# Performance work log

Measured on AMD Instinct MI355X. Metric: run time of the kernel, lower is better.

Reference implementation:

```python
import jax, jax.numpy as jnp
import numpy as np

DIM = 256
NUM_HEADS = 8
HEAD_DIM = DIM // NUM_HEADS
KERNEL_SIZES = (5, 7, 9)
DILATIONS = (1, 2, 3)
HEADS_PER_RANGE = (4, 3, 1)  # replicates torch allocation: weights~1/k^2, floor + greedy remainder
SCALE = HEAD_DIM ** -0.5


def _unfold(x, ks, dil):
    # x: (B, h, d, H, W) -> (B, h, d, L, H, W), L = ks*ks, same-padded dilated neighborhood gather
    B, h, d, H, W = x.shape
    pad = (ks // 2) * dil
    xp = jnp.pad(x, ((0, 0), (0, 0), (0, 0), (pad, pad), (pad, pad)))
    patches = [xp[..., i * dil:i * dil + H, j * dil:j * dil + W]
               for i in range(ks) for j in range(ks)]
    return jnp.stack(patches, axis=3)


def _attend_range(q, k, v, ks, dil, rpb):
    # q,k,v: (B, h_i, d, H, W); rpb: (h_i, L)
    k_nb = _unfold(k, ks, dil)  # (B,h,d,L,H,W)
    v_nb = _unfold(v, ks, dil)
    logits = jnp.einsum('bhdxy,bhdlxy->bhlxy', q * SCALE, k_nb)
    logits = logits + rpb[None, :, :, None, None]
    attn = jax.nn.softmax(logits, axis=2)
    return jnp.einsum('bhlxy,bhdlxy->bhdxy', attn, v_nb)


def setup_inputs() -> dict:
    key = jax.random.key(0)
    ks = jax.random.split(key, 6)
    B, C, H, W = 4, DIM, 64, 64
    s = 0.02
    inp = {
        'x': jax.random.normal(ks[0], (B, C, H, W), dtype=jnp.float32),
        'qkv_w': jax.random.normal(ks[1], (3 * DIM, DIM), dtype=jnp.float32) * s,
        'qkv_b': jnp.zeros((3 * DIM,), dtype=jnp.float32),
        'proj_w': jax.random.normal(ks[2], (DIM, DIM), dtype=jnp.float32) * s,
        'proj_b': jnp.zeros((DIM,), dtype=jnp.float32),
    }
    for i, kk in enumerate(KERNEL_SIZES):
        inp[f'rpb{i}'] = jax.random.normal(ks[3 + i], (HEADS_PER_RANGE[i], kk * kk), dtype=jnp.float32) * s
    return inp


def reference(x, qkv_w, qkv_b, proj_w, proj_b, rpb0, rpb1, rpb2):
    B, C, H, W = x.shape
    qkv = jnp.einsum('oc,bcxy->boxy', qkv_w, x) + qkv_b[None, :, None, None]
    q, k, v = jnp.split(qkv, 3, axis=1)
    q = q.reshape(B, NUM_HEADS, HEAD_DIM, H, W)
    k = k.reshape(B, NUM_HEADS, HEAD_DIM, H, W)
    v = v.reshape(B, NUM_HEADS, HEAD_DIM, H, W)
    rpbs = (rpb0, rpb1, rpb2)
    outs = []
    hs = 0
    for i in range(len(KERNEL_SIZES)):
        he = hs + HEADS_PER_RANGE[i]
        outs.append(_attend_range(q[:, hs:he], k[:, hs:he], v[:, hs:he],
                                  KERNEL_SIZES[i], DILATIONS[i], rpbs[i]))
        hs = he
    out = jnp.concatenate(outs, axis=1).reshape(B, C, H, W)
    out = jnp.einsum('oc,bcxy->boxy', proj_w, out) + proj_b[None, :, None, None]
    return out
```

## Files before the change

kernel.cpp:

```cpp
#include <hip/hip_runtime.h>
#include <math.h>

#define H_IMG 64
#define W_IMG 64
#define PIX   (H_IMG * W_IMG)
#define NB    4
#define NHEADS 8
#define HD    32
#define CDIM  256
#define QKV_C 768
#define ATT_SCALE 0.17677669529663687f

typedef _Float16 half8_t __attribute__((ext_vector_type(8)));
typedef _Float16 half2_t __attribute__((ext_vector_type(2)));
typedef float f32x4 __attribute__((ext_vector_type(4)));

__global__ void cvt_w16(const float* __restrict__ a, int na,
                        const float* __restrict__ b, int nb,
                        _Float16* __restrict__ da, _Float16* __restrict__ db) {
    int i = blockIdx.x * 256 + threadIdx.x;
    if (i < na) da[i] = (_Float16)a[i];
    else if (i - na < nb) db[i - na] = (_Float16)b[i - na];
}

__launch_bounds__(256)
__global__ void transpose_to_f16(const float* __restrict__ src,
                                 _Float16* __restrict__ dst, int C) {
    __shared__ _Float16 tl[64][66];
    const int b  = blockIdx.z;
    const int p0 = blockIdx.x * 64;
    const int c0 = blockIdx.y * 64;
    const int tx = threadIdx.x;
    const int ty = threadIdx.y;
    const float* s = src + (size_t)b * C * PIX;
    _Float16* d = dst + (size_t)b * PIX * C;
#pragma unroll
    for (int cc = ty; cc < 64; cc += 4)
        tl[cc][tx] = (_Float16)s[(size_t)(c0 + cc) * PIX + p0 + tx];
    __syncthreads();
#pragma unroll
    for (int pp = ty; pp < 64; pp += 4)
        d[(size_t)(p0 + pp) * C + c0 + tx] = tl[tx][pp];
}

template <typename OutT, bool PAIR>
__launch_bounds__(256)
__global__ void gemm16(const _Float16* __restrict__ A,
                       const _Float16* __restrict__ BT,
                       const float* __restrict__ bias,
                       OutT* __restrict__ Y,
                       int M, int K, int N) {
    __shared__ _Float16 Asl[128][40];
    __shared__ _Float16 Bsl[128][40];
    const int b = blockIdx.z;
    const _Float16* Bb = BT + (size_t)b * N * K;
    OutT* Yb = Y + (size_t)b * M * N;
    const int m0 = blockIdx.y * 128;
    const int n0 = blockIdx.x * 128;
    const int t    = threadIdx.x;
    const int lane = t & 63;
    const int w    = t >> 6;
    const int wm = w >> 1, wn = w & 1;
    const int l15 = lane & 15;
    const int kq  = (lane >> 4) * 8;

    f32x4 acc[4][4];
#pragma unroll
    for (int mt = 0; mt < 4; mt++)
#pragma unroll
        for (int nt = 0; nt < 4; nt++)
            acc[mt][nt] = (f32x4){0.f, 0.f, 0.f, 0.f};

    for (int k0 = 0; k0 < K; k0 += 32) {
        __syncthreads();
#pragma unroll
        for (int i = 0; i < 2; i++) {
            int idx = t + i * 256;
            int row = idx >> 2;
            int seg = (idx & 3) * 8;
            *(half8_t*)&Asl[row][seg] = *(const half8_t*)(A  + (size_t)(m0 + row) * K + k0 + seg);
            *(half8_t*)&Bsl[row][seg] = *(const half8_t*)(Bb + (size_t)(n0 + row) * K + k0 + seg);
        }
        __syncthreads();
        half8_t af[4], bf[4];
#pragma unroll
        for (int mt = 0; mt < 4; mt++)
            af[mt] = *(const half8_t*)&Asl[wm * 64 + mt * 16 + l15][kq];
#pragma unroll
        for (int nt = 0; nt < 4; nt++)
            bf[nt] = *(const half8_t*)&Bsl[wn * 64 + nt * 16 + l15][kq];
#pragma unroll
        for (int mt = 0; mt < 4; mt++)
#pragma unroll
            for (int nt = 0; nt < 4; nt++)
                acc[mt][nt] = __builtin_amdgcn_mfma_f32_16x16x32_f16(
                    af[mt], bf[nt], acc[mt][nt], 0, 0, 0);
    }

    const int rq = lane >> 4;
    if constexpr (PAIR) {
        unsigned* Yp = (unsigned*)Yb;
#pragma unroll
        for (int mt = 0; mt < 4; mt++) {
#pragma unroll
            for (int s = 0; s < 2; s++) {
                int mp = m0 + wm * 64 + mt * 16 + rq * 4 + 2 * s;
                float b0 = bias[mp], b1 = bias[mp + 1];
#pragma unroll
                for (int nt = 0; nt < 4; nt++) {
                    int col = n0 + wn * 64 + nt * 16 + l15;
                    half2_t hv;
                    hv.x = (_Float16)(acc[mt][nt][2 * s]     + b0);
                    hv.y = (_Float16)(acc[mt][nt][2 * s + 1] + b1);
                    Yp[(size_t)(mp >> 1) * N + col] = __builtin_bit_cast(unsigned, hv);
                }
            }
        }
    } else {
#pragma unroll
        for (int mt = 0; mt < 4; mt++) {
#pragma unroll
            for (int r = 0; r < 4; r++) {
                int m = m0 + wm * 64 + mt * 16 + rq * 4 + r;
                float bs = bias[m];
                OutT* yp = Yb + (size_t)m * N + n0 + wn * 64;
#pragma unroll
                for (int nt = 0; nt < 4; nt++)
                    yp[nt * 16 + l15] = (OutT)(acc[mt][nt][r] + bs);
            }
        }
    }
}

template <int KS, int DIL>
__device__ __forceinline__ void attn_part(const unsigned* __restrict__ base,
                                          const float* __restrict__ rp,
                                          int h, int y, int i0, int i1,
                                          float* __restrict__ acc,
                                          float& denom) {
    const int x = threadIdx.x;

    const unsigned* qb = base + (size_t)(h * 16) * PIX + y * W_IMG + x;
    const unsigned* kb = base + (size_t)(128 + h * 16) * PIX + x;
    const unsigned* vb = base + (size_t)(256 + h * 16) * PIX + x;

    half2_t qh[16];
#pragma unroll
    for (int d2 = 0; d2 < 16; d2++)
        qh[d2] = __builtin_bit_cast(half2_t, qb[(size_t)d2 * PIX]);

#pragma unroll 1
    for (int i = i0; i < i1; i++) {
        const int yy = y + (i - KS / 2) * DIL;
        const float* rrow = rp + i * KS;
        if ((unsigned)yy < (unsigned)H_IMG) {
            int kr[16], vr[16];
            const unsigned* ko = kb + yy * W_IMG;
            const unsigned* vo = vb + yy * W_IMG;
#pragma unroll
            for (int d2 = 0; d2 < 16; d2++) {
                kr[d2] = (int)ko[(size_t)d2 * PIX];
                vr[d2] = (int)vo[(size_t)d2 * PIX];
            }
#pragma unroll
            for (int j = 0; j < KS; j++) {
                const int xx = x + (j - KS / 2) * DIL;
                const int src = xx & 63;
                const bool vx = (unsigned)xx < (unsigned)W_IMG;
                float s0 = 0.f, s1 = 0.f, s2 = 0.f, s3 = 0.f;
#pragma unroll
                for (int d2 = 0; d2 < 16; d2 += 4) {
                    half2_t k0 = __builtin_bit_cast(half2_t, __shfl(kr[d2 + 0], src));
                    half2_t k1 = __builtin_bit_cast(half2_t, __shfl(kr[d2 + 1], src));
                    half2_t k2 = __builtin_bit_cast(half2_t, __shfl(kr[d2 + 2], src));
                    half2_t k3 = __builtin_bit_cast(half2_t, __shfl(kr[d2 + 3], src));
#if __has_builtin(__builtin_amdgcn_fdot2)
                    s0 = __builtin_amdgcn_fdot2(qh[d2 + 0], k0, s0, false);
                    s1 = __builtin_amdgcn_fdot2(qh[d2 + 1], k1, s1, false);
                    s2 = __builtin_amdgcn_fdot2(qh[d2 + 2], k2, s2, false);
                    s3 = __builtin_amdgcn_fdot2(qh[d2 + 3], k3, s3, false);
#else
                    s0 += (float)qh[d2+0].x * (float)k0.x + (float)qh[d2+0].y * (float)k0.y;
                    s1 += (float)qh[d2+1].x * (float)k1.x + (float)qh[d2+1].y * (float)k1.y;
                    s2 += (float)qh[d2+2].x * (float)k2.x + (float)qh[d2+2].y * (float)k2.y;
                    s3 += (float)qh[d2+3].x * (float)k3.x + (float)qh[d2+3].y * (float)k3.y;
#endif
                }
                const float rb = rrow[j];
                float logit = fmaf((s0 + s1) + (s2 + s3), ATT_SCALE, rb);
                logit = vx ? logit : rb;
                const float wgt = __expf(logit);
                denom += wgt;
                const float wv = vx ? wgt : 0.f;
#pragma unroll
                for (int d2 = 0; d2 < 16; d2++) {
                    half2_t vv = __builtin_bit_cast(half2_t, __shfl(vr[d2], src));
                    acc[2 * d2]     += wv * (float)vv.x;
                    acc[2 * d2 + 1] += wv * (float)vv.y;
                }
            }
        } else {
#pragma unroll
            for (int j = 0; j < KS; j++) denom += __expf(rrow[j]);
        }
    }
}

__device__ __forceinline__ void store_attn(_Float16* __restrict__ op,
                                           const float* __restrict__ acc,
                                           float denom) {
    const float inv = 1.f / denom;
#pragma unroll
    for (int g = 0; g < 4; g++) {
        half8_t hv;
#pragma unroll
        for (int e = 0; e < 8; e++) hv[e] = (_Float16)(acc[g * 8 + e] * inv);
        *(half8_t*)(op + g * 8) = hv;
    }
}

__launch_bounds__(832)
__global__ void attn_v5(const unsigned* __restrict__ qkv,
                        const float* __restrict__ rpb0,
                        const float* __restrict__ rpb1,
                        const float* __restrict__ rpb2,
                        _Float16* __restrict__ outT) {
    __shared__ float P[9][33][64];
    const int b  = blockIdx.x;
    const int y  = blockIdx.y;
    const int x  = threadIdx.x;
    const int ty = threadIdx.y;

    const unsigned* base = qkv + (size_t)b * (QKV_C / 2) * PIX;
    const int p = y * W_IMG + x;

    float acc[HD];
#pragma unroll
    for (int d = 0; d < HD; d++) acc[d] = 0.f;
    float denom = 0.f;

    int h;
    int slot = -1;
    if (ty < 4) {
        h = ty;
        attn_part<5, 1>(base, rpb0 + h * 25, h, y, 0, 5, acc, denom);
    } else if (ty < 10) {
        const int idx = ty - 4;
        h = 4 + (idx >> 1);
        const int half = idx & 1;
        attn_part<7, 2>(base, rpb1 + (h - 4) * 49, h, y, half ? 4 : 0, half ? 7 : 4, acc, denom);
        slot = idx;
    } else {
        h = 7;
        const int t3 = ty - 10;
        attn_part<9, 3>(base, rpb2, h, y, 3 * t3, 3 * t3 + 3, acc, denom);
        slot = 6 + t3;
    }

    _Float16* op = outT + ((size_t)b * PIX + p) * CDIM + h * HD;

    if (slot < 0) {
        store_attn(op, acc, denom);
    } else {
#pragma unroll
        for (int d = 0; d < HD; d++) P[slot][d][x] = acc[d];
        P[slot][HD][x] = denom;
    }
    __syncthreads();

    if (ty == 4 || ty == 6 || ty == 8) {
        const int s0 = ty - 4;
        float m[HD];
#pragma unroll
        for (int d = 0; d < HD; d++) m[d] = P[s0][d][x] + P[s0 + 1][d][x];
        store_attn(op, m, P[s0][HD][x] + P[s0 + 1][HD][x]);
    } else if (ty == 10) {
        float m[HD];
#pragma unroll
        for (int d = 0; d < HD; d++) m[d] = P[6][d][x] + P[7][d][x] + P[8][d][x];
        store_attn(op, m, P[6][HD][x] + P[7][HD][x] + P[8][HD][x]);
    }
}

extern "C" void kernel_launch(void* const* d_in, const int* in_sizes, int n_in,
                              void* d_out, int out_size, void* d_ws, size_t ws_size,
                              hipStream_t stream) {
    const float* x      = (const float*)d_in[0];
    const float* qkv_w  = (const float*)d_in[1];
    const float* qkv_b  = (const float*)d_in[2];
    const float* proj_w = (const float*)d_in[3];
    const float* proj_b = (const float*)d_in[4];
    const float* rpb0   = (const float*)d_in[5];
    const float* rpb1   = (const float*)d_in[6];
    const float* rpb2   = (const float*)d_in[7];
    float* out = (float*)d_out;

    char* ws = (char*)d_ws;
    _Float16* qkv16 = (_Float16*)ws;
    _Float16* T16   = (_Float16*)(ws + (size_t)NB * QKV_C * PIX * 2);
    _Float16* W16   = T16 + (size_t)NB * PIX * CDIM;
    _Float16* P16   = W16 + (size_t)QKV_C * CDIM;

    const int nw = QKV_C * CDIM, np = CDIM * CDIM;
    cvt_w16<<<dim3((nw + np + 255) / 256), dim3(256), 0, stream>>>(qkv_w, nw, proj_w, np, W16, P16);

    transpose_to_f16<<<dim3(PIX / 64, CDIM / 64, NB), dim3(64, 4), 0, stream>>>(x, T16, CDIM);

    gemm16<_Float16, true><<<dim3(PIX / 128, QKV_C / 128, NB), dim3(256), 0, stream>>>(
        W16, T16, qkv_b, qkv16, QKV_C, CDIM, PIX);

    attn_v5<<<dim3(NB, H_IMG), dim3(64, 13), 0, stream>>>(
        (const unsigned*)qkv16, rpb0, rpb1, rpb2, T16);

    gemm16<float, false><<<dim3(PIX / 128, CDIM / 128, NB), dim3(256), 0, stream>>>(
        P16, T16, proj_b, out, CDIM, CDIM, PIX);
}
```

Baseline: 152.6 us.

## Fuse weight conversion into transpose kernel and load V neighbors directly

Merges the weight fp32-to-fp16 conversion into the input transpose kernel as an extra z-slice of blocks, removing one kernel launch. In the attention loop, V values for each neighbor are now loaded directly from global memory at the clamped column instead of being held per row and broadcast with cross-lane shuffles. This trades shuffle instructions and register pressure for more global/cache loads per neighbor.

```diff
diff --git a/kernel.cpp b/kernel.cpp
--- a/kernel.cpp
+++ b/kernel.cpp
@@ -15,32 +15,36 @@
 typedef _Float16 half2_t __attribute__((ext_vector_type(2)));
 typedef float f32x4 __attribute__((ext_vector_type(4)));
 
-__global__ void cvt_w16(const float* __restrict__ a, int na,
-                        const float* __restrict__ b, int nb,
-                        _Float16* __restrict__ da, _Float16* __restrict__ db) {
-    int i = blockIdx.x * 256 + threadIdx.x;
-    if (i < na) da[i] = (_Float16)a[i];
-    else if (i - na < nb) db[i - na] = (_Float16)b[i - na];
-}
-
 __launch_bounds__(256)
-__global__ void transpose_to_f16(const float* __restrict__ src,
-                                 _Float16* __restrict__ dst, int C) {
+__global__ void transpose_cvt(const float* __restrict__ src, _Float16* __restrict__ dst,
+                              const float* __restrict__ w1, int n1,
+                              const float* __restrict__ w2, int n2,
+                              _Float16* __restrict__ d1, _Float16* __restrict__ d2) {
+    const int tx = threadIdx.x;
+    const int ty = threadIdx.y;
+    if (blockIdx.z == NB) {
+        const int bid = blockIdx.y * 64 + blockIdx.x;
+        int tid = bid * 256 + ty * 64 + tx;
+        const int total = n1 + n2;
+        for (int i = tid; i < total; i += 65536) {
+            if (i < n1) d1[i] = (_Float16)w1[i];
+            else        d2[i - n1] = (_Float16)w2[i - n1];
+        }
+        return;
+    }
     __shared__ _Float16 tl[64][66];
     const int b  = blockIdx.z;
     const int p0 = blockIdx.x * 64;
     const int c0 = blockIdx.y * 64;
-    const int tx = threadIdx.x;
-    const int ty = threadIdx.y;
-    const float* s = src + (size_t)b * C * PIX;
-    _Float16* d = dst + (size_t)b * PIX * C;
+    const float* s = src + (size_t)b * CDIM * PIX;
+    _Float16* d = dst + (size_t)b * PIX * CDIM;
 #pragma unroll
     for (int cc = ty; cc < 64; cc += 4)
         tl[cc][tx] = (_Float16)s[(size_t)(c0 + cc) * PIX + p0 + tx];
     __syncthreads();
 #pragma unroll
     for (int pp = ty; pp < 64; pp += 4)
-        d[(size_t)(p0 + pp) * C + c0 + tx] = tl[tx][pp];
+        d[(size_t)(p0 + pp) * CDIM + c0 + tx] = tl[tx][pp];
 }
 
 template <typename OutT, bool PAIR>
@@ -142,7 +146,7 @@
 
     const unsigned* qb = base + (size_t)(h * 16) * PIX + y * W_IMG + x;
     const unsigned* kb = base + (size_t)(128 + h * 16) * PIX + x;
-    const unsigned* vb = base + (size_t)(256 + h * 16) * PIX + x;
+    const unsigned* vb = base + (size_t)(256 + h * 16) * PIX;
 
     half2_t qh[16];
 #pragma unroll
@@ -154,19 +158,22 @@
         const int yy = y + (i - KS / 2) * DIL;
         const float* rrow = rp + i * KS;
         if ((unsigned)yy < (unsigned)H_IMG) {
-            int kr[16], vr[16];
+            int kr[16];
             const unsigned* ko = kb + yy * W_IMG;
-            const unsigned* vo = vb + yy * W_IMG;
-#pragma unroll
-            for (int d2 = 0; d2 < 16; d2++) {
+#pragma unroll
+            for (int d2 = 0; d2 < 16; d2++)
                 kr[d2] = (int)ko[(size_t)d2 * PIX];
-                vr[d2] = (int)vo[(size_t)d2 * PIX];
-            }
+            const unsigned* vrow = vb + yy * W_IMG;
 #pragma unroll
             for (int j = 0; j < KS; j++) {
                 const int xx = x + (j - KS / 2) * DIL;
                 const int src = xx & 63;
                 const bool vx = (unsigned)xx < (unsigned)W_IMG;
+                const int xc = xx < 0 ? 0 : (xx > 63 ? 63 : xx);
+                unsigned vld[16];
+#pragma unroll
+                for (int d2 = 0; d2 < 16; d2++)
+                    vld[d2] = vrow[(size_t)d2 * PIX + xc];
                 float s0 = 0.f, s1 = 0.f, s2 = 0.f, s3 = 0.f;
 #pragma unroll
                 for (int d2 = 0; d2 < 16; d2 += 4) {
@@ -194,7 +201,7 @@
                 const float wv = vx ? wgt : 0.f;
 #pragma unroll
                 for (int d2 = 0; d2 < 16; d2++) {
-                    half2_t vv = __builtin_bit_cast(half2_t, __shfl(vr[d2], src));
+                    half2_t vv = __builtin_bit_cast(half2_t, vld[d2]);
                     acc[2 * d2]     += wv * (float)vv.x;
                     acc[2 * d2 + 1] += wv * (float)vv.y;
                 }
@@ -220,7 +227,7 @@
 }
 
 __launch_bounds__(832)
-__global__ void attn_v5(const unsigned* __restrict__ qkv,
+__global__ void attn_v6(const unsigned* __restrict__ qkv,
                         const float* __restrict__ rpb0,
                         const float* __restrict__ rpb1,
                         const float* __restrict__ rpb2,
@@ -302,14 +309,14 @@
     _Float16* P16   = W16 + (size_t)QKV_C * CDIM;
 
     const int nw = QKV_C * CDIM, np = CDIM * CDIM;
-    cvt_w16<<<dim3((nw + np + 255) / 256), dim3(256), 0, stream>>>(qkv_w, nw, proj_w, np, W16, P16);
-
-    transpose_to_f16<<<dim3(PIX / 64, CDIM / 64, NB), dim3(64, 4), 0, stream>>>(x, T16, CDIM);
+
+    transpose_cvt<<<dim3(PIX / 64, CDIM / 64, NB + 1), dim3(64, 4), 0, stream>>>(
+        x, T16, qkv_w, nw, proj_w, np, W16, P16);
 
     gemm16<_Float16, true><<<dim3(PIX / 128, QKV_C / 128, NB), dim3(256), 0, stream>>>(
         W16, T16, qkv_b, qkv16, QKV_C, CDIM, PIX);
 
-    attn_v5<<<dim3(NB, H_IMG), dim3(64, 13), 0, stream>>>(
+    attn_v6<<<dim3(NB, H_IMG), dim3(64, 13), 0, stream>>>(
         (const unsigned*)qkv16, rpb0, rpb1, rpb2, T16);
 
     gemm16<float, false><<<dim3(PIX / 128, CDIM / 128, NB), dim3(256), 0, stream>>>(
```

Measured after the change: 229.1 us. 1.5x slower.
